# Optimization experiments

Measured on AMD Instinct MI355X. Metric: run time of the kernel, lower is better.

## Reference

```python
import jax, jax.numpy as jnp
import numpy as np

FILTER_SIZE = 7
SIGMA = 1.5
K1 = 0.01
K2 = 0.03
MAX_VAL = 1.0
CHANNEL = 1


def _gaussian_kernel3d(size, channel, sigma):
    coords = jnp.arange(size, dtype=jnp.float32) - (size - 1.0) / 2.0
    g = -(coords ** 2) / (2.0 * sigma ** 2)
    # grid[i,j,k] = g[j] + g[i] + g[k], matching torch view(1,-1,1)+view(-1,1,1)+view(1,1,-1)
    grid = g[None, :, None] + g[:, None, None] + g[None, None, :]
    grid = jax.nn.softmax(grid.reshape(-1))
    kernel = grid.reshape(1, 1, size, size, size)
    return jnp.broadcast_to(kernel, (channel, 1, size, size, size))


def _dwconv3d(x, kernel, channel):
    # depthwise (groups=channel) valid conv, NCDHW
    return jax.lax.conv_general_dilated(
        x, kernel, window_strides=(1, 1, 1), padding='VALID',
        dimension_numbers=('NCDHW', 'OIDHW', 'NCDHW'),
        feature_group_count=channel)


def setup_inputs() -> dict:
    key = jax.random.key(0)
    k1, k2 = jax.random.split(key)
    shape = (2, 1, 192, 192, 192)
    return {
        'input': jax.random.uniform(k1, shape, dtype=jnp.float32),
        'target': jax.random.uniform(k2, shape, dtype=jnp.float32),
    }


def reference(input, target):
    kernel = _gaussian_kernel3d(FILTER_SIZE, CHANNEL, SIGMA)
    c1 = (K1 * MAX_VAL) ** 2
    c2 = (K2 * MAX_VAL) ** 2
    mu1 = _dwconv3d(input, kernel, CHANNEL)
    mu2 = _dwconv3d(target, kernel, CHANNEL)
    mu1_sq = mu1 * mu1
    mu2_sq = mu2 * mu2
    mu1_mu2 = mu1 * mu2
    sigma1_sq = _dwconv3d(input * input, kernel, CHANNEL) - mu1_sq
    sigma2_sq = _dwconv3d(target * target, kernel, CHANNEL) - mu2_sq
    sigma12 = _dwconv3d(input * target, kernel, CHANNEL) - mu1_mu2
    v1 = 2.0 * sigma12 + c2
    v2 = sigma1_sq + sigma2_sq + c2
    ssim = (2.0 * mu1_mu2 + c1) * v1 / ((mu1_sq + mu2_sq + c1) * v2)
    return jnp.mean(ssim)  # reduction='mean'
```

## Files before the change

kernel.cpp:

```cpp
#include <hip/hip_runtime.h>
#include <utility>


#define DIMS 192
#define OD   186
#define VOL  (DIMS * DIMS * DIMS)
#define ZCH  32
#define NZT  6
#define XCH  27
#define NCHX 7
#define NP   (XCH + 6)
#define YT   8
#define YIN  14

#define ZP_P   15
#define ZP_F   (ZCH * ZP_P)
#define YP_P   9
#define YP_F   (ZCH * YP_P)
#define YP_OFF (5 * ZP_F)
#define LDS_N  (YP_OFF + 5 * YP_F)

#define NBLK   (NZT * 24 * NCHX * 2)

#define AI __attribute__((always_inline))

__global__ __launch_bounds__(256, 4)
void ssim3d_kernel(const float* __restrict__ X, const float* __restrict__ Y,
                   double* __restrict__ acc_out, unsigned* __restrict__ cnt,
                   float* __restrict__ out) {
    __shared__ float lds[LDS_N];
    __shared__ float wsum[4];
    const int tid = threadIdx.x;

    float w[7];
    {
        float s = 0.f;
        #pragma unroll
        for (int t = 0; t < 7; ++t) {
            float d = (float)t - 3.0f;
            w[t] = expf(-d * d / 4.5f);
            s += w[t];
        }
        #pragma unroll
        for (int t = 0; t < 7; ++t)
            w[t] = __uint_as_float(__builtin_amdgcn_readfirstlane(__float_as_uint(w[t] / s)));
    }

    const int L  = blockIdx.x + NZT * (blockIdx.y + 24 * blockIdx.z);
    const int v  = (L & 7) * (NBLK / 8) + (L >> 3);
    const int cb = v / 144;
    const int rem = v - cb * 144;
    const int by  = rem % 24;
    const int bz  = rem / 24;
    const int cx  = cb % NCHX;
    const int n   = cb / NCHX;

    const int z0 = bz * ZCH;
    const int y0 = by * YT;
    const int x0 = cx * XCH;

    const float* Xb = X + (size_t)n * VOL;
    const float* Yb = Y + (size_t)n * VOL;

    const int zj = tid >> 4;
    const int zs = tid & 15;
    const bool zact = (zj < YIN);
    const int zc = z0 + zs * 2;
    const int gy = min(y0 + zj, DIMS - 1);
    const unsigned rowoff = (unsigned)gy * DIMS + (unsigned)zc;
    const bool ztail = (zc + 7 > DIMS - 1);

    const int bfld = tid >> 5;
    const int bk   = tid & 31;
    const bool bact = (bfld < 5);

    const int aj = tid >> 5;
    const int ak = tid & 31;
    const bool av = (z0 + ak < OD) && (y0 + aj < OD);
    const int xmax = OD + 6 - x0;

    float acc[7][5];
    #pragma unroll
    for (int q = 0; q < 7; ++q)
        #pragma unroll
        for (int m = 0; m < 5; ++m) acc[q][m] = 0.f;

    float lsum = 0.f;
    const float c1 = 1e-4f, c2 = 9e-4f;

    float pfx[8], pfy[8];

    auto loadX = [&](int xi) AI {
        if (!zact) return;
        int gx = min(x0 + xi, DIMS - 1);
        const float* p = Xb + (size_t)gx * (DIMS * DIMS);
        if (!ztail) {
            const float* q = p + rowoff;
            #pragma unroll
            for (int t = 0; t < 4; ++t) {
                float2 a = *(const float2*)(q + 2 * t);
                pfx[2 * t] = a.x; pfx[2 * t + 1] = a.y;
            }
        } else {
            unsigned ro = (unsigned)gy * DIMS;
            #pragma unroll
            for (int j = 0; j < 8; ++j)
                pfx[j] = p[ro + (unsigned)min(zc + j, DIMS - 1)];
        }
    };
    auto loadY = [&](int xi) AI {
        if (!zact) return;
        int gx = min(x0 + xi, DIMS - 1);
        const float* p = Yb + (size_t)gx * (DIMS * DIMS);
        if (!ztail) {
            const float* q = p + rowoff;
            #pragma unroll
            for (int t = 0; t < 4; ++t) {
                float2 a = *(const float2*)(q + 2 * t);
                pfy[2 * t] = a.x; pfy[2 * t + 1] = a.y;
            }
        } else {
            unsigned ro = (unsigned)gy * DIMS;
            #pragma unroll
            for (int j = 0; j < 8; ++j)
                pfy[j] = p[ro + (unsigned)min(zc + j, DIMS - 1)];
        }
    };

    auto ssim_pt = [&](float mu1, float mu2, float ex2, float ey2, float exy) AI {
        float mu11 = mu1 * mu1, mu22 = mu2 * mu2, mu12 = mu1 * mu2;
        float num = (2.f * mu12 + c1) * (2.f * (exy - mu12) + c2);
        float den = (mu11 + mu22 + c1) * ((ex2 - mu11) + (ey2 - mu22) + c2);
        lsum += num * __builtin_amdgcn_rcpf(den);
    };

    auto body = [&](int xi, auto ucell) AI {
        constexpr int U = decltype(ucell)::value;

        if (zact) {
            #pragma unroll
            for (int o = 0; o < 2; ++o) {
                float a0 = 0.f, a1 = 0.f, a2 = 0.f, a3 = 0.f, a4 = 0.f;
                #pragma unroll
                for (int t = 0; t < 7; ++t) {
                    float xx = pfx[o + t], yy = pfy[o + t], wt = w[t];
                    a0 += wt * xx;
                    a1 += wt * yy;
                    a2 += wt * (xx * xx);
                    a3 += wt * (yy * yy);
                    a4 += wt * (xx * yy);
                }
                int b = (zs * 2 + o) * ZP_P + zj;
                lds[b]            = a0;
                lds[b + ZP_F]     = a1;
                lds[b + 2 * ZP_F] = a2;
                lds[b + 3 * ZP_F] = a3;
                lds[b + 4 * ZP_F] = a4;
            }
        }
        if (xi + 1 < NP) loadX(xi + 1);
        __syncthreads();

        if (bact) {
            const float* src = &lds[bfld * ZP_F + bk * ZP_P];
            float vy[YIN];
            #pragma unroll
            for (int jj = 0; jj < YIN; ++jj) vy[jj] = src[jj];
            float* dst = &lds[YP_OFF + bfld * YP_F + bk * YP_P];
            #pragma unroll
            for (int j = 0; j < YT; ++j) {
                float a = 0.f;
                #pragma unroll
                for (int tt = 0; tt < 7; ++tt) a += w[tt] * vy[j + tt];
                dst[j] = a;
            }
        }
        if (xi + 1 < NP) loadY(xi + 1);
        __syncthreads();

        float vv[5];
        #pragma unroll
        for (int f = 0; f < 5; ++f)
            vv[f] = lds[YP_OFF + f * YP_F + ak * YP_P + aj];
        #pragma unroll
        for (int d = 0; d < 7; ++d) {
            float wq = w[d];
            #pragma unroll
            for (int m = 0; m < 5; ++m)
                acc[(U + 7 - d) % 7][m] += wq * vv[m];
        }
        constexpr int sc = (U + 1) % 7;
        if (xi >= 6 && xi < xmax && av)
            ssim_pt(acc[sc][0], acc[sc][1], acc[sc][2], acc[sc][3], acc[sc][4]);
        #pragma unroll
        for (int m = 0; m < 5; ++m) acc[sc][m] = 0.f;
    };

    loadX(0); loadY(0);
    #pragma unroll 1
    for (int b = 0; b < 28; b += 7) {
        body(b + 0, std::integral_constant<int, 0>{});
        body(b + 1, std::integral_constant<int, 1>{});
        body(b + 2, std::integral_constant<int, 2>{});
        body(b + 3, std::integral_constant<int, 3>{});
        body(b + 4, std::integral_constant<int, 4>{});
        body(b + 5, std::integral_constant<int, 5>{});
        body(b + 6, std::integral_constant<int, 6>{});
    }
    body(28, std::integral_constant<int, 0>{});
    body(29, std::integral_constant<int, 1>{});
    body(30, std::integral_constant<int, 2>{});
    body(31, std::integral_constant<int, 3>{});
    body(32, std::integral_constant<int, 4>{});

    #pragma unroll
    for (int off = 32; off > 0; off >>= 1) lsum += __shfl_down(lsum, off, 64);
    if ((tid & 63) == 0) wsum[tid >> 6] = lsum;
    __syncthreads();
    if (tid == 0) {
        double bs = (double)(wsum[0] + wsum[1] + wsum[2] + wsum[3]);
        atomicAdd(acc_out, bs);
        __threadfence();
        unsigned prev = atomicAdd(cnt, 1u);
        if (prev == (unsigned)(NBLK - 1)) {
            double tot = atomicAdd(acc_out, 0.0);
            out[0] = (float)(tot / 12869712.0);
        }
    }
}

extern "C" void kernel_launch(void* const* d_in, const int* in_sizes, int n_in,
                              void* d_out, int out_size, void* d_ws, size_t ws_size,
                              hipStream_t stream) {
    (void)in_sizes; (void)n_in; (void)out_size; (void)ws_size;
    const float* x = (const float*)d_in[0];
    const float* y = (const float*)d_in[1];
    double* acc = (double*)d_ws;
    unsigned* cnt = (unsigned*)((char*)d_ws + 8);
    hipMemsetAsync(d_ws, 0, 16, stream);
    dim3 grid(NZT, 24, NCHX * 2);
    ssim3d_kernel<<<grid, 256, 0, stream>>>(x, y, acc, cnt, (float*)d_out);
}
```

Baseline: 293.4 us.

## Fuse y-pass into accumulation stage and double-buffer LDS to drop a barrier

The separate y-convolution stage, which wrote y-filtered planes to a second LDS region, is removed. Each thread now computes its own 7-tap y-filter directly from the z-filtered LDS plane for its output point. The z-plane buffer is double-buffered by x parity so one __syncthreads per x step is enough, and the X and Y prefetches are issued together. The price is more LDS reads and FMAs per thread (35 reads instead of 5, with redundant y-filtering across threads) in exchange for one fewer barrier and one fewer LDS write/read round.

```diff
diff --git a/kernel.cpp b/kernel.cpp
--- a/kernel.cpp
+++ b/kernel.cpp
@@ -13,12 +13,10 @@
 #define YT   8
 #define YIN  14
 
-#define ZP_P   15
-#define ZP_F   (ZCH * ZP_P)
-#define YP_P   9
-#define YP_F   (ZCH * YP_P)
-#define YP_OFF (5 * ZP_F)
-#define LDS_N  (YP_OFF + 5 * YP_F)
+#define ZP_P    15
+#define ZP_F    (ZCH * ZP_P)
+#define ZP_HALF (5 * ZP_F)
+#define LDS_N   (2 * ZP_HALF)
 
 #define NBLK   (NZT * 24 * NCHX * 2)
 
@@ -70,10 +68,6 @@
     const unsigned rowoff = (unsigned)gy * DIMS + (unsigned)zc;
     const bool ztail = (zc + 7 > DIMS - 1);
 
-    const int bfld = tid >> 5;
-    const int bk   = tid & 31;
-    const bool bact = (bfld < 5);
-
     const int aj = tid >> 5;
     const int ak = tid & 31;
     const bool av = (z0 + ak < OD) && (y0 + aj < OD);
@@ -136,6 +130,7 @@
 
     auto body = [&](int xi, auto ucell) AI {
         constexpr int U = decltype(ucell)::value;
+        float* zp = &lds[(xi & 1) * ZP_HALF];
 
         if (zact) {
             #pragma unroll
@@ -151,43 +146,31 @@
                     a4 += wt * (xx * yy);
                 }
                 int b = (zs * 2 + o) * ZP_P + zj;
-                lds[b]            = a0;
-                lds[b + ZP_F]     = a1;
-                lds[b + 2 * ZP_F] = a2;
-                lds[b + 3 * ZP_F] = a3;
-                lds[b + 4 * ZP_F] = a4;
+                zp[b]            = a0;
+                zp[b + ZP_F]     = a1;
+                zp[b + 2 * ZP_F] = a2;
+                zp[b + 3 * ZP_F] = a3;
+                zp[b + 4 * ZP_F] = a4;
             }
         }
-        if (xi + 1 < NP) loadX(xi + 1);
+        if (xi + 1 < NP) { loadX(xi + 1); loadY(xi + 1); }
         __syncthreads();
 
-        if (bact) {
-            const float* src = &lds[bfld * ZP_F + bk * ZP_P];
-            float vy[YIN];
-            #pragma unroll
-            for (int jj = 0; jj < YIN; ++jj) vy[jj] = src[jj];
-            float* dst = &lds[YP_OFF + bfld * YP_F + bk * YP_P];
-            #pragma unroll
-            for (int j = 0; j < YT; ++j) {
-                float a = 0.f;
-                #pragma unroll
-                for (int tt = 0; tt < 7; ++tt) a += w[tt] * vy[j + tt];
-                dst[j] = a;
-            }
-        }
-        if (xi + 1 < NP) loadY(xi + 1);
-        __syncthreads();
-
-        float vv[5];
-        #pragma unroll
-        for (int f = 0; f < 5; ++f)
-            vv[f] = lds[YP_OFF + f * YP_F + ak * YP_P + aj];
+        float yv[5];
+        #pragma unroll
+        for (int f = 0; f < 5; ++f) {
+            const float* src = &zp[f * ZP_F + ak * ZP_P + aj];
+            float a = 0.f;
+            #pragma unroll
+            for (int ty = 0; ty < 7; ++ty) a += w[ty] * src[ty];
+            yv[f] = a;
+        }
         #pragma unroll
         for (int d = 0; d < 7; ++d) {
             float wq = w[d];
             #pragma unroll
             for (int m = 0; m < 5; ++m)
-                acc[(U + 7 - d) % 7][m] += wq * vv[m];
+                acc[(U + 7 - d) % 7][m] += wq * yv[m];
         }
         constexpr int sc = (U + 1) % 7;
         if (xi >= 6 && xi < xmax && av)
```

Result: slower. 347.5 us (+18.4%).

## Enlarge SSIM tiles to 48z x 47x with 512-thread blocks

Applied to the files above, without the earlier changes.

Each block now covers a larger z chunk (48 instead of 32) and x chunk (47 instead of 27) and uses 512 threads, with the thread-to-work mappings for each convolution stage remapped to match. The larger tiles reduce the share of halo reloads and redundant z/y convolution work along x and z, and cut the number of blocks and atomics. The block-to-tile mapping is simplified to a bitwise decode. In exchange the block holds more LDS, runs with inactive lanes in several stages, and may reach lower occupancy and have fewer blocks to balance across CUs.

```diff
diff --git a/kernel.cpp b/kernel.cpp
--- a/kernel.cpp
+++ b/kernel.cpp
@@ -5,10 +5,10 @@
 #define DIMS 192
 #define OD   186
 #define VOL  (DIMS * DIMS * DIMS)
-#define ZCH  32
-#define NZT  6
-#define XCH  27
-#define NCHX 7
+#define ZCH  48
+#define NZT  4
+#define XCH  47
+#define NCHX 4
 #define NP   (XCH + 6)
 #define YT   8
 #define YIN  14
@@ -16,7 +16,7 @@
 #define ZP_P   15
 #define ZP_F   (ZCH * ZP_P)
 #define YP_P   9
-#define YP_F   (ZCH * YP_P)
+#define YP_F   (64 * YP_P)
 #define YP_OFF (5 * ZP_F)
 #define LDS_N  (YP_OFF + 5 * YP_F)
 
@@ -24,12 +24,12 @@
 
 #define AI __attribute__((always_inline))
 
-__global__ __launch_bounds__(256, 4)
+__global__ __launch_bounds__(512, 6)
 void ssim3d_kernel(const float* __restrict__ X, const float* __restrict__ Y,
                    double* __restrict__ acc_out, unsigned* __restrict__ cnt,
                    float* __restrict__ out) {
     __shared__ float lds[LDS_N];
-    __shared__ float wsum[4];
+    __shared__ float wsum[8];
     const int tid = threadIdx.x;
 
     float w[7];
@@ -46,14 +46,13 @@
             w[t] = __uint_as_float(__builtin_amdgcn_readfirstlane(__float_as_uint(w[t] / s)));
     }
 
-    const int L  = blockIdx.x + NZT * (blockIdx.y + 24 * blockIdx.z);
-    const int v  = (L & 7) * (NBLK / 8) + (L >> 3);
-    const int cb = v / 144;
-    const int rem = v - cb * 144;
+    const int L   = blockIdx.x + NZT * (blockIdx.y + 24 * blockIdx.z);
+    const int cb  = L & 7;
+    const int rem = L >> 3;
     const int by  = rem % 24;
     const int bz  = rem / 24;
-    const int cx  = cb % NCHX;
-    const int n   = cb / NCHX;
+    const int cx  = cb & 3;
+    const int n   = cb >> 2;
 
     const int z0 = bz * ZCH;
     const int y0 = by * YT;
@@ -62,21 +61,21 @@
     const float* Xb = X + (size_t)n * VOL;
     const float* Yb = Y + (size_t)n * VOL;
 
-    const int zj = tid >> 4;
-    const int zs = tid & 15;
-    const bool zact = (zj < YIN);
+    const int zj = tid >> 5;
+    const int zs = tid & 31;
+    const bool zact = (zj < YIN) && (zs < 24);
     const int zc = z0 + zs * 2;
     const int gy = min(y0 + zj, DIMS - 1);
     const unsigned rowoff = (unsigned)gy * DIMS + (unsigned)zc;
     const bool ztail = (zc + 7 > DIMS - 1);
 
-    const int bfld = tid >> 5;
-    const int bk   = tid & 31;
-    const bool bact = (bfld < 5);
-
-    const int aj = tid >> 5;
-    const int ak = tid & 31;
-    const bool av = (z0 + ak < OD) && (y0 + aj < OD);
+    const int bf = tid >> 6;
+    const int bk = tid & 63;
+    const bool bact = (bf < 5) && (bk < 48);
+
+    const int aj = tid >> 6;
+    const int ak = tid & 63;
+    const bool av = (ak < ZCH) && (z0 + ak < OD) && (y0 + aj < OD);
     const int xmax = OD + 6 - x0;
 
     float acc[7][5];
@@ -162,11 +161,11 @@
         __syncthreads();
 
         if (bact) {
-            const float* src = &lds[bfld * ZP_F + bk * ZP_P];
+            const float* src = &lds[bf * ZP_F + bk * ZP_P];
             float vy[YIN];
             #pragma unroll
             for (int jj = 0; jj < YIN; ++jj) vy[jj] = src[jj];
-            float* dst = &lds[YP_OFF + bfld * YP_F + bk * YP_P];
+            float* dst = &lds[YP_OFF + bf * YP_F + bk * YP_P];
             #pragma unroll
             for (int j = 0; j < YT; ++j) {
                 float a = 0.f;
@@ -198,7 +197,7 @@
 
     loadX(0); loadY(0);
     #pragma unroll 1
-    for (int b = 0; b < 28; b += 7) {
+    for (int b = 0; b < 49; b += 7) {
         body(b + 0, std::integral_constant<int, 0>{});
         body(b + 1, std::integral_constant<int, 1>{});
         body(b + 2, std::integral_constant<int, 2>{});
@@ -207,19 +206,20 @@
         body(b + 5, std::integral_constant<int, 5>{});
         body(b + 6, std::integral_constant<int, 6>{});
     }
-    body(28, std::integral_constant<int, 0>{});
-    body(29, std::integral_constant<int, 1>{});
-    body(30, std::integral_constant<int, 2>{});
-    body(31, std::integral_constant<int, 3>{});
-    body(32, std::integral_constant<int, 4>{});
+    body(49, std::integral_constant<int, 0>{});
+    body(50, std::integral_constant<int, 1>{});
+    body(51, std::integral_constant<int, 2>{});
+    body(52, std::integral_constant<int, 3>{});
 
     #pragma unroll
     for (int off = 32; off > 0; off >>= 1) lsum += __shfl_down(lsum, off, 64);
     if ((tid & 63) == 0) wsum[tid >> 6] = lsum;
     __syncthreads();
     if (tid == 0) {
-        double bs = (double)(wsum[0] + wsum[1] + wsum[2] + wsum[3]);
-        atomicAdd(acc_out, bs);
+        float bsf = 0.f;
+        #pragma unroll
+        for (int q = 0; q < 8; ++q) bsf += wsum[q];
+        atomicAdd(acc_out, (double)bsf);
         __threadfence();
         unsigned prev = atomicAdd(cnt, 1u);
         if (prev == (unsigned)(NBLK - 1)) {
@@ -239,5 +239,5 @@
     unsigned* cnt = (unsigned*)((char*)d_ws + 8);
     hipMemsetAsync(d_ws, 0, 16, stream);
     dim3 grid(NZT, 24, NCHX * 2);
-    ssim3d_kernel<<<grid, 256, 0, stream>>>(x, y, acc, cnt, (float*)d_out);
+    ssim3d_kernel<<<grid, 512, 0, stream>>>(x, y, acc, cnt, (float*)d_out);
 }
```

Result: slower. 611.2 us (+108.3%).
